# Kernel tuning notes

Hardware: AMD Instinct MI355X
Metric: run time of the kernel (lower is better)

Reference implementation:

```python
import jax, jax.numpy as jnp
import numpy as np

T = 2.0          # temperature (hardcoded to 2 in the torch module)
EPSILON = 0.1    # sinkhorn entropic regularization
N_ITERS = 10     # sinkhorn_loss default n_iters
CLIP_MAX = 10.0  # torch.clamp(Wxy, max=10.0)
EPS = 1e-8
LOSS_SCALE = 0.001


def setup_inputs() -> dict:
    key = jax.random.key(0)
    k1, k2 = jax.random.split(key)
    B, N, D = 4, 256, 512
    y_s = jax.random.normal(k1, (B, N, D), dtype=jnp.float32)
    y_t = jax.random.normal(k2, (B, N, D), dtype=jnp.float32)
    return {"y_s": y_s, "y_t": y_t}


def _sinkhorn_sample(x, y):
    # x, y: [N, D] probability rows. L1 cost matrix [N, N].
    W = jnp.sum(jnp.abs(x[:, None, :] - y[None, :, :]), axis=-1)
    Wc = jnp.minimum(W, CLIP_MAX)
    K = jnp.exp(-Wc / EPSILON) + EPS  # x = x + 1e-8 before normalization

    def step(P, _):
        P = P / jnp.maximum(jnp.sum(P, axis=1, keepdims=True), EPS)
        P = P / jnp.maximum(jnp.sum(P, axis=0, keepdims=True), EPS)
        return P, None

    P, _ = jax.lax.scan(step, K, None, length=N_ITERS)
    return jnp.sum(P * W)


def reference(y_s, y_t):
    p_s = jax.nn.softmax(y_s / T, axis=-1)
    p_t = jax.nn.softmax(y_t / T, axis=-1)
    losses = jax.vmap(_sinkhorn_sample)(p_s, p_t)  # [B]
    # emd_loss = sum_i 0.001 * loss_i; returned value = emd_loss / B
    return LOSS_SCALE * jnp.mean(losses)
```

## Files before the change

kernel.cpp:

```cpp
#include <hip/hip_runtime.h>

#define NB 4
#define NN 256
#define ND 512
#define NITER 10

typedef __attribute__((ext_vector_type(8))) unsigned short ushort8v;

__device__ __forceinline__ unsigned short f2bf(float x) {
  unsigned u = __float_as_uint(x);
  u += 0x7fffu + ((u >> 16) & 1u);
  return (unsigned short)(u >> 16);
}
__device__ __forceinline__ float bf2f(unsigned short h) {
  return __uint_as_float(((unsigned)h) << 16);
}

__global__ __launch_bounds__(256) void softmax_k(const float* __restrict__ ys,
                                                 const float* __restrict__ yt,
                                                 float* __restrict__ ps,
                                                 float* __restrict__ pt) {
  int bb = blockIdx.x;
  const float* src = (bb < NB * NN) ? ys : yt;
  float* dst       = (bb < NB * NN) ? ps : pt;
  int row = bb & (NB * NN - 1);
  const float* rp = src + (size_t)row * ND;
  float* wp = dst + (size_t)row * ND;
  int t = threadIdx.x;
  float a = rp[t];
  float b = rp[t + 256];
  float m = fmaxf(a, b);
  #pragma unroll
  for (int s = 1; s < 64; s <<= 1) m = fmaxf(m, __shfl_xor(m, s));
  __shared__ float red[4];
  int wid = t >> 6;
  if ((t & 63) == 0) red[wid] = m;
  __syncthreads();
  m = fmaxf(fmaxf(red[0], red[1]), fmaxf(red[2], red[3]));
  float e0 = expf((a - m) * 0.5f);
  float e1 = expf((b - m) * 0.5f);
  float ssum = e0 + e1;
  #pragma unroll
  for (int s = 1; s < 64; s <<= 1) ssum += __shfl_xor(ssum, s);
  __syncthreads();
  if ((t & 63) == 0) red[wid] = ssum;
  __syncthreads();
  ssum = red[0] + red[1] + red[2] + red[3];
  float inv = 1.0f / ssum;
  wp[t] = e0 * inv;
  wp[t + 256] = e1 * inv;
}

__global__ __launch_bounds__(256) void cost_k(const float* __restrict__ ps,
                                              const float* __restrict__ pt,
                                              float* __restrict__ W) {
  __shared__ float xs[32 * 512];
  __shared__ float ysh[32 * 512];
  int b  = blockIdx.z;
  int It = blockIdx.y * 32;
  int Jt = blockIdx.x * 32;
  int t = threadIdx.x;
  const float4* xg = reinterpret_cast<const float4*>(ps + ((size_t)b * NN + It) * ND);
  const float4* yg = reinterpret_cast<const float4*>(pt + ((size_t)b * NN + Jt) * ND);
  float4* xsv = reinterpret_cast<float4*>(xs);
  float4* ysv = reinterpret_cast<float4*>(ysh);
  #pragma unroll
  for (int s = 0; s < 16; ++s) {
    int idx = s * 256 + t;
    int r = idx >> 7;
    int q = idx & 127;
    int qs = q ^ ((r >> 1) & 7);
    xsv[r * 128 + qs] = xg[idx];
    ysv[r * 128 + qs] = yg[idx];
  }
  __syncthreads();
  int tx = t & 15, ty = t >> 4;
  int i0 = ty * 2, j0 = tx * 2;
  int sx = ty & 7;
  int sy = tx & 7;
  float a00 = 0.f, a01 = 0.f, a10 = 0.f, a11 = 0.f;
  for (int q = 0; q < 128; ++q) {
    float4 x0 = xsv[i0 * 128 + (q ^ sx)];
    float4 x1 = xsv[(i0 + 1) * 128 + (q ^ sx)];
    float4 y0 = ysv[j0 * 128 + (q ^ sy)];
    float4 y1 = ysv[(j0 + 1) * 128 + (q ^ sy)];
    a00 += fabsf(x0.x - y0.x) + fabsf(x0.y - y0.y) + fabsf(x0.z - y0.z) + fabsf(x0.w - y0.w);
    a01 += fabsf(x0.x - y1.x) + fabsf(x0.y - y1.y) + fabsf(x0.z - y1.z) + fabsf(x0.w - y1.w);
    a10 += fabsf(x1.x - y0.x) + fabsf(x1.y - y0.y) + fabsf(x1.z - y0.z) + fabsf(x1.w - y0.w);
    a11 += fabsf(x1.x - y1.x) + fabsf(x1.y - y1.y) + fabsf(x1.z - y1.z) + fabsf(x1.w - y1.w);
  }
  size_t base = ((size_t)b * NN + It + i0) * NN + Jt + j0;
  W[base]          = a00;  W[base + 1]      = a01;
  W[base + NN]     = a10;  W[base + NN + 1] = a11;
}

__global__ __launch_bounds__(1024) void sink_k(const float* __restrict__ Wg,
                                               float* __restrict__ losses) {
  __shared__ __align__(16) unsigned short Kl[NN * NN];
  __shared__ __align__(16) float u[NN];
  __shared__ __align__(16) float v[NN];
  __shared__ __align__(16) float scr[8 * NN];
  int b = blockIdx.x;
  int t = threadIdx.x;
  const float4* W4 = reinterpret_cast<const float4*>(Wg + (size_t)b * NN * NN);

  #pragma unroll
  for (int s = 0; s < 16; ++s) {
    int q = s * 1024 + t;
    int e = q * 4;
    int i = e >> 8;
    int j = e & 255;
    float4 w4 = W4[q];
    float k0 = __expf(fminf(w4.x, 10.0f) * -10.0f) + 1e-8f;
    float k1 = __expf(fminf(w4.y, 10.0f) * -10.0f) + 1e-8f;
    float k2 = __expf(fminf(w4.z, 10.0f) * -10.0f) + 1e-8f;
    float k3 = __expf(fminf(w4.w, 10.0f) * -10.0f) + 1e-8f;
    int pj = j ^ ((i & 7) << 3);
    ushort4 kk;
    kk.x = f2bf(k0); kk.y = f2bf(k1); kk.z = f2bf(k2); kk.w = f2bf(k3);
    *reinterpret_cast<ushort4*>(&Kl[i * 256 + pj]) = kk;
  }
  if (t < NN) { u[t] = 1.0f; v[t] = 1.0f; }
  __syncthreads();

  for (int it = 0; it < NITER; ++it) {
    {
      int i = t & 255, c = t >> 8;
      const int rowb = i * 256;
      const int sw = (i & 7) << 3;
      float acc = 0.0f;
      #pragma unroll
      for (int q = 0; q < 8; ++q) {
        int j0 = c * 64 + q * 8;
        float4 va = *reinterpret_cast<const float4*>(&v[j0]);
        float4 vb = *reinterpret_cast<const float4*>(&v[j0 + 4]);
        ushort8v k8 = *reinterpret_cast<const ushort8v*>(&Kl[rowb + (j0 ^ sw)]);
        acc += bf2f(k8[0]) * va.x + bf2f(k8[1]) * va.y +
               bf2f(k8[2]) * va.z + bf2f(k8[3]) * va.w +
               bf2f(k8[4]) * vb.x + bf2f(k8[5]) * vb.y +
               bf2f(k8[6]) * vb.z + bf2f(k8[7]) * vb.w;
      }
      scr[c * 256 + i] = acc;
    }
    __syncthreads();
    if (t < NN) {
      float r = scr[t] + scr[256 + t] + scr[512 + t] + scr[768 + t];
      float uo = u[t];
      u[t] = uo / fmaxf(uo * r, 1e-8f);
    }
    __syncthreads();
    {
      int j2 = t & 127, c = t >> 7;
      float acc0 = 0.0f, acc1 = 0.0f;
      #pragma unroll
      for (int q = 0; q < 8; ++q) {
        int ib = c * 32 + q * 4;
        float4 uq = *reinterpret_cast<const float4*>(&u[ib]);
        {
          int i = ib + 0;
          unsigned dw = *reinterpret_cast<const unsigned*>(&Kl[i * 256 + ((2 * j2) ^ ((i & 7) << 3))]);
          acc0 += __uint_as_float(dw << 16) * uq.x;
          acc1 += __uint_as_float(dw & 0xffff0000u) * uq.x;
        }
        {
          int i = ib + 1;
          unsigned dw = *reinterpret_cast<const unsigned*>(&Kl[i * 256 + ((2 * j2) ^ ((i & 7) << 3))]);
          acc0 += __uint_as_float(dw << 16) * uq.y;
          acc1 += __uint_as_float(dw & 0xffff0000u) * uq.y;
        }
        {
          int i = ib + 2;
          unsigned dw = *reinterpret_cast<const unsigned*>(&Kl[i * 256 + ((2 * j2) ^ ((i & 7) << 3))]);
          acc0 += __uint_as_float(dw << 16) * uq.z;
          acc1 += __uint_as_float(dw & 0xffff0000u) * uq.z;
        }
        {
          int i = ib + 3;
          unsigned dw = *reinterpret_cast<const unsigned*>(&Kl[i * 256 + ((2 * j2) ^ ((i & 7) << 3))]);
          acc0 += __uint_as_float(dw << 16) * uq.w;
          acc1 += __uint_as_float(dw & 0xffff0000u) * uq.w;
        }
      }
      *reinterpret_cast<float2*>(&scr[c * 256 + 2 * j2]) = make_float2(acc0, acc1);
    }
    __syncthreads();
    if (t < NN) {
      float s0 = 0.0f;
      #pragma unroll
      for (int c = 0; c < 8; ++c) s0 += scr[c * 256 + t];
      float vo = v[t];
      v[t] = vo / fmaxf(vo * s0, 1e-8f);
    }
    __syncthreads();
  }

  float acc = 0.0f;
  #pragma unroll
  for (int s = 0; s < 16; ++s) {
    int q = s * 1024 + t;
    int e = q * 4;
    int i = e >> 8;
    int j = e & 255;
    float4 w4 = W4[q];
    int pj = j ^ ((i & 7) << 3);
    ushort4 k4 = *reinterpret_cast<const ushort4*>(&Kl[i * 256 + pj]);
    float4 v4 = *reinterpret_cast<const float4*>(&v[j]);
    float ui = u[i];
    acc += ui * (bf2f(k4.x) * v4.x * w4.x + bf2f(k4.y) * v4.y * w4.y +
                 bf2f(k4.z) * v4.z * w4.z + bf2f(k4.w) * v4.w * w4.w);
  }
  #pragma unroll
  for (int s = 1; s < 64; s <<= 1) acc += __shfl_xor(acc, s);
  __syncthreads();
  if ((t & 63) == 0) scr[t >> 6] = acc;
  __syncthreads();
  if (t == 0) {
    float tot = 0.0f;
    #pragma unroll
    for (int w = 0; w < 16; ++w) tot += scr[w];
    losses[b] = tot;
  }
}

__global__ void final_k(const float* __restrict__ losses, float* __restrict__ out) {
  if (threadIdx.x == 0 && blockIdx.x == 0) {
    out[0] = 0.001f * 0.25f * (losses[0] + losses[1] + losses[2] + losses[3]);
  }
}

extern "C" void kernel_launch(void* const* d_in, const int* in_sizes, int n_in,
                              void* d_out, int out_size, void* d_ws, size_t ws_size,
                              hipStream_t stream) {
  const float* ys = (const float*)d_in[0];
  const float* yt = (const float*)d_in[1];
  float* ws = (float*)d_ws;
  float* ps = ws;
  float* pt = ps + (size_t)NB * NN * ND;
  float* W  = pt + (size_t)NB * NN * ND;
  float* losses = W + (size_t)NB * NN * NN;
  float* out = (float*)d_out;

  softmax_k<<<2 * NB * NN, 256, 0, stream>>>(ys, yt, ps, pt);
  cost_k<<<dim3(8, 8, NB), 256, 0, stream>>>(ps, pt, W);
  sink_k<<<NB, 1024, 0, stream>>>(W, losses);
  final_k<<<1, 64, 0, stream>>>(losses, out);
}
```

Measured before the change: 112.7 us.

## Store softmax and cost matrix in fp16, drop final kernel via atomicAdd

Softmax outputs and the L1 cost matrix are now stored as fp16 instead of fp32, halving global and LDS traffic in the cost and sinkhorn kernels. The cost kernel uses 8-wide half vectors with a rotation-based LDS swizzle. The column-sum pass in sinkhorn is repartitioned into 16 chunks of 4 columns each. The final reduction kernel is removed: output is zeroed in softmax and each sinkhorn block atomically adds its scaled loss. The trade-off is fp16 rounding of probabilities and of cost values up to ~2, which perturbs exp(-10W) and the loss sum.

```diff
diff --git a/kernel.cpp b/kernel.cpp
--- a/kernel.cpp
+++ b/kernel.cpp
@@ -5,7 +5,10 @@
 #define ND 512
 #define NITER 10
 
+typedef _Float16 half_t;
 typedef __attribute__((ext_vector_type(8))) unsigned short ushort8v;
+typedef __attribute__((ext_vector_type(8))) _Float16 half8v;
+typedef __attribute__((ext_vector_type(2))) _Float16 half2v;
 
 __device__ __forceinline__ unsigned short f2bf(float x) {
   unsigned u = __float_as_uint(x);
@@ -18,14 +21,16 @@
 
 __global__ __launch_bounds__(256) void softmax_k(const float* __restrict__ ys,
                                                  const float* __restrict__ yt,
-                                                 float* __restrict__ ps,
-                                                 float* __restrict__ pt) {
+                                                 half_t* __restrict__ ps,
+                                                 half_t* __restrict__ pt,
+                                                 float* __restrict__ out) {
   int bb = blockIdx.x;
+  if (bb == 0 && threadIdx.x == 0) out[0] = 0.0f;
   const float* src = (bb < NB * NN) ? ys : yt;
-  float* dst       = (bb < NB * NN) ? ps : pt;
+  half_t* dst      = (bb < NB * NN) ? ps : pt;
   int row = bb & (NB * NN - 1);
   const float* rp = src + (size_t)row * ND;
-  float* wp = dst + (size_t)row * ND;
+  half_t* wp = dst + (size_t)row * ND;
   int t = threadIdx.x;
   float a = rp[t];
   float b = rp[t + 256];
@@ -47,78 +52,88 @@
   __syncthreads();
   ssum = red[0] + red[1] + red[2] + red[3];
   float inv = 1.0f / ssum;
-  wp[t] = e0 * inv;
-  wp[t + 256] = e1 * inv;
-}
-
-__global__ __launch_bounds__(256) void cost_k(const float* __restrict__ ps,
-                                              const float* __restrict__ pt,
-                                              float* __restrict__ W) {
-  __shared__ float xs[32 * 512];
-  __shared__ float ysh[32 * 512];
+  wp[t]       = (half_t)(e0 * inv);
+  wp[t + 256] = (half_t)(e1 * inv);
+}
+
+__global__ __launch_bounds__(256) void cost_k(const half_t* __restrict__ ps,
+                                              const half_t* __restrict__ pt,
+                                              half_t* __restrict__ W) {
+  __shared__ half_t xs[32 * 512];
+  __shared__ half_t ysh[32 * 512];
   int b  = blockIdx.z;
   int It = blockIdx.y * 32;
   int Jt = blockIdx.x * 32;
   int t = threadIdx.x;
-  const float4* xg = reinterpret_cast<const float4*>(ps + ((size_t)b * NN + It) * ND);
-  const float4* yg = reinterpret_cast<const float4*>(pt + ((size_t)b * NN + Jt) * ND);
-  float4* xsv = reinterpret_cast<float4*>(xs);
-  float4* ysv = reinterpret_cast<float4*>(ysh);
-  #pragma unroll
-  for (int s = 0; s < 16; ++s) {
-    int idx = s * 256 + t;
-    int r = idx >> 7;
-    int q = idx & 127;
-    int qs = q ^ ((r >> 1) & 7);
-    xsv[r * 128 + qs] = xg[idx];
-    ysv[r * 128 + qs] = yg[idx];
+  const half8v* xg = reinterpret_cast<const half8v*>(ps + ((size_t)b * NN + It) * ND);
+  const half8v* yg = reinterpret_cast<const half8v*>(pt + ((size_t)b * NN + Jt) * ND);
+  half8v* xsv = reinterpret_cast<half8v*>(xs);
+  half8v* ysv = reinterpret_cast<half8v*>(ysh);
+  #pragma unroll
+  for (int s = 0; s < 8; ++s) {
+    int qidx = s * 256 + t;
+    int r = qidx >> 6;
+    int q = qidx & 63;
+    int rot = (r + (r >> 3)) & 7;
+    int dst = r * 64 + ((q + rot) & 63);
+    xsv[dst] = xg[qidx];
+    ysv[dst] = yg[qidx];
   }
   __syncthreads();
   int tx = t & 15, ty = t >> 4;
-  int i0 = ty * 2, j0 = tx * 2;
-  int sx = ty & 7;
-  int sy = tx & 7;
+  int i0 = 2 * ty, j0 = 2 * tx;
+  int rx0 = (i0 + (i0 >> 3)) & 7;
+  int rx1 = ((i0 + 1) + ((i0 + 1) >> 3)) & 7;
+  int ry0 = (j0 + (j0 >> 3)) & 7;
+  int ry1 = ((j0 + 1) + ((j0 + 1) >> 3)) & 7;
   float a00 = 0.f, a01 = 0.f, a10 = 0.f, a11 = 0.f;
-  for (int q = 0; q < 128; ++q) {
-    float4 x0 = xsv[i0 * 128 + (q ^ sx)];
-    float4 x1 = xsv[(i0 + 1) * 128 + (q ^ sx)];
-    float4 y0 = ysv[j0 * 128 + (q ^ sy)];
-    float4 y1 = ysv[(j0 + 1) * 128 + (q ^ sy)];
-    a00 += fabsf(x0.x - y0.x) + fabsf(x0.y - y0.y) + fabsf(x0.z - y0.z) + fabsf(x0.w - y0.w);
-    a01 += fabsf(x0.x - y1.x) + fabsf(x0.y - y1.y) + fabsf(x0.z - y1.z) + fabsf(x0.w - y1.w);
-    a10 += fabsf(x1.x - y0.x) + fabsf(x1.y - y0.y) + fabsf(x1.z - y0.z) + fabsf(x1.w - y0.w);
-    a11 += fabsf(x1.x - y1.x) + fabsf(x1.y - y1.y) + fabsf(x1.z - y1.z) + fabsf(x1.w - y1.w);
-  }
-  size_t base = ((size_t)b * NN + It + i0) * NN + Jt + j0;
-  W[base]          = a00;  W[base + 1]      = a01;
-  W[base + NN]     = a10;  W[base + NN + 1] = a11;
-}
-
-__global__ __launch_bounds__(1024) void sink_k(const float* __restrict__ Wg,
-                                               float* __restrict__ losses) {
+  #pragma unroll 4
+  for (int qq = 0; qq < 64; ++qq) {
+    half8v x0 = xsv[i0 * 64 + ((qq + rx0) & 63)];
+    half8v x1 = xsv[(i0 + 1) * 64 + ((qq + rx1) & 63)];
+    half8v y0 = ysv[j0 * 64 + ((qq + ry0) & 63)];
+    half8v y1 = ysv[(j0 + 1) * 64 + ((qq + ry1) & 63)];
+    #pragma unroll
+    for (int e = 0; e < 8; ++e) {
+      float xf0 = (float)x0[e], xf1 = (float)x1[e];
+      float yf0 = (float)y0[e], yf1 = (float)y1[e];
+      a00 += fabsf(xf0 - yf0);
+      a01 += fabsf(xf0 - yf1);
+      a10 += fabsf(xf1 - yf0);
+      a11 += fabsf(xf1 - yf1);
+    }
+  }
+  half_t* wb = W + ((size_t)b * NN + It + i0) * NN + Jt + j0;
+  half2v w0; w0[0] = (half_t)a00; w0[1] = (half_t)a01;
+  half2v w1; w1[0] = (half_t)a10; w1[1] = (half_t)a11;
+  *reinterpret_cast<half2v*>(wb)      = w0;
+  *reinterpret_cast<half2v*>(wb + NN) = w1;
+}
+
+__global__ __launch_bounds__(1024) void sink_k(const half_t* __restrict__ Wg,
+                                               float* __restrict__ out) {
   __shared__ __align__(16) unsigned short Kl[NN * NN];
   __shared__ __align__(16) float u[NN];
   __shared__ __align__(16) float v[NN];
-  __shared__ __align__(16) float scr[8 * NN];
+  __shared__ __align__(16) float scr[16 * NN];
   int b = blockIdx.x;
   int t = threadIdx.x;
-  const float4* W4 = reinterpret_cast<const float4*>(Wg + (size_t)b * NN * NN);
-
-  #pragma unroll
-  for (int s = 0; s < 16; ++s) {
-    int q = s * 1024 + t;
-    int e = q * 4;
+  const half8v* W8 = reinterpret_cast<const half8v*>(Wg + (size_t)b * NN * NN);
+
+  #pragma unroll
+  for (int s = 0; s < 8; ++s) {
+    int q8 = s * 1024 + t;
+    int e = q8 * 8;
     int i = e >> 8;
     int j = e & 255;
-    float4 w4 = W4[q];
-    float k0 = __expf(fminf(w4.x, 10.0f) * -10.0f) + 1e-8f;
-    float k1 = __expf(fminf(w4.y, 10.0f) * -10.0f) + 1e-8f;
-    float k2 = __expf(fminf(w4.z, 10.0f) * -10.0f) + 1e-8f;
-    float k3 = __expf(fminf(w4.w, 10.0f) * -10.0f) + 1e-8f;
-    int pj = j ^ ((i & 7) << 3);
-    ushort4 kk;
-    kk.x = f2bf(k0); kk.y = f2bf(k1); kk.z = f2bf(k2); kk.w = f2bf(k3);
-    *reinterpret_cast<ushort4*>(&Kl[i * 256 + pj]) = kk;
+    half8v w8 = W8[q8];
+    ushort8v kk;
+    #pragma unroll
+    for (int r = 0; r < 8; ++r) {
+      float kf = __expf(fminf((float)w8[r], 10.0f) * -10.0f) + 1e-8f;
+      kk[r] = f2bf(kf);
+    }
+    *reinterpret_cast<ushort8v*>(&Kl[i * 256 + (j ^ ((i & 7) << 3))]) = kk;
   }
   if (t < NN) { u[t] = 1.0f; v[t] = 1.0f; }
   __syncthreads();
@@ -150,44 +165,45 @@
     }
     __syncthreads();
     {
-      int j2 = t & 127, c = t >> 7;
-      float acc0 = 0.0f, acc1 = 0.0f;
+      int j4 = t & 63, c = t >> 6;
+      int jc = 4 * j4;
+      float acc0 = 0.f, acc1 = 0.f, acc2 = 0.f, acc3 = 0.f;
       #pragma unroll
-      for (int q = 0; q < 8; ++q) {
-        int ib = c * 32 + q * 4;
+      for (int q4 = 0; q4 < 4; ++q4) {
+        int ib = c * 16 + q4 * 4;
         float4 uq = *reinterpret_cast<const float4*>(&u[ib]);
         {
           int i = ib + 0;
-          unsigned dw = *reinterpret_cast<const unsigned*>(&Kl[i * 256 + ((2 * j2) ^ ((i & 7) << 3))]);
-          acc0 += __uint_as_float(dw << 16) * uq.x;
-          acc1 += __uint_as_float(dw & 0xffff0000u) * uq.x;
+          ushort4 k4 = *reinterpret_cast<const ushort4*>(&Kl[i * 256 + (jc ^ ((i & 7) << 3))]);
+          acc0 += bf2f(k4.x) * uq.x; acc1 += bf2f(k4.y) * uq.x;
+          acc2 += bf2f(k4.z) * uq.x; acc3 += bf2f(k4.w) * uq.x;
         }
         {
           int i = ib + 1;
-          unsigned dw = *reinterpret_cast<const unsigned*>(&Kl[i * 256 + ((2 * j2) ^ ((i & 7) << 3))]);
-          acc0 += __uint_as_float(dw << 16) * uq.y;
-          acc1 += __uint_as_float(dw & 0xffff0000u) * uq.y;
+          ushort4 k4 = *reinterpret_cast<const ushort4*>(&Kl[i * 256 + (jc ^ ((i & 7) << 3))]);
+          acc0 += bf2f(k4.x) * uq.y; acc1 += bf2f(k4.y) * uq.y;
+          acc2 += bf2f(k4.z) * uq.y; acc3 += bf2f(k4.w) * uq.y;
         }
         {
           int i = ib + 2;
-          unsigned dw = *reinterpret_cast<const unsigned*>(&Kl[i * 256 + ((2 * j2) ^ ((i & 7) << 3))]);
-          acc0 += __uint_as_float(dw << 16) * uq.z;
-          acc1 += __uint_as_float(dw & 0xffff0000u) * uq.z;
+          ushort4 k4 = *reinterpret_cast<const ushort4*>(&Kl[i * 256 + (jc ^ ((i & 7) << 3))]);
+          acc0 += bf2f(k4.x) * uq.z; acc1 += bf2f(k4.y) * uq.z;
+          acc2 += bf2f(k4.z) * uq.z; acc3 += bf2f(k4.w) * uq.z;
         }
         {
           int i = ib + 3;
-          unsigned dw = *reinterpret_cast<const unsigned*>(&Kl[i * 256 + ((2 * j2) ^ ((i & 7) << 3))]);
-          acc0 += __uint_as_float(dw << 16) * uq.w;
-          acc1 += __uint_as_float(dw & 0xffff0000u) * uq.w;
+          ushort4 k4 = *reinterpret_cast<const ushort4*>(&Kl[i * 256 + (jc ^ ((i & 7) << 3))]);
+          acc0 += bf2f(k4.x) * uq.w; acc1 += bf2f(k4.y) * uq.w;
+          acc2 += bf2f(k4.z) * uq.w; acc3 += bf2f(k4.w) * uq.w;
         }
       }
-      *reinterpret_cast<float2*>(&scr[c * 256 + 2 * j2]) = make_float2(acc0, acc1);
+      *reinterpret_cast<float4*>(&scr[c * 256 + jc]) = make_float4(acc0, acc1, acc2, acc3);
     }
     __syncthreads();
     if (t < NN) {
       float s0 = 0.0f;
       #pragma unroll
-      for (int c = 0; c < 8; ++c) s0 += scr[c * 256 + t];
+      for (int c = 0; c < 16; ++c) s0 += scr[c * 256 + t];
       float vo = v[t];
       v[t] = vo / fmaxf(vo * s0, 1e-8f);
     }
@@ -196,18 +212,20 @@
 
   float acc = 0.0f;
   #pragma unroll
-  for (int s = 0; s < 16; ++s) {
-    int q = s * 1024 + t;
-    int e = q * 4;
+  for (int s = 0; s < 8; ++s) {
+    int q8 = s * 1024 + t;
+    int e = q8 * 8;
     int i = e >> 8;
     int j = e & 255;
-    float4 w4 = W4[q];
-    int pj = j ^ ((i & 7) << 3);
-    ushort4 k4 = *reinterpret_cast<const ushort4*>(&Kl[i * 256 + pj]);
-    float4 v4 = *reinterpret_cast<const float4*>(&v[j]);
+    half8v w8 = W8[q8];
+    ushort8v k8 = *reinterpret_cast<const ushort8v*>(&Kl[i * 256 + (j ^ ((i & 7) << 3))]);
     float ui = u[i];
-    acc += ui * (bf2f(k4.x) * v4.x * w4.x + bf2f(k4.y) * v4.y * w4.y +
-                 bf2f(k4.z) * v4.z * w4.z + bf2f(k4.w) * v4.w * w4.w);
+    float4 v0 = *reinterpret_cast<const float4*>(&v[j]);
+    float4 v1 = *reinterpret_cast<const float4*>(&v[j + 4]);
+    acc += ui * (bf2f(k8[0]) * v0.x * (float)w8[0] + bf2f(k8[1]) * v0.y * (float)w8[1] +
+                 bf2f(k8[2]) * v0.z * (float)w8[2] + bf2f(k8[3]) * v0.w * (float)w8[3] +
+                 bf2f(k8[4]) * v1.x * (float)w8[4] + bf2f(k8[5]) * v1.y * (float)w8[5] +
+                 bf2f(k8[6]) * v1.z * (float)w8[6] + bf2f(k8[7]) * v1.w * (float)w8[7]);
   }
   #pragma unroll
   for (int s = 1; s < 64; s <<= 1) acc += __shfl_xor(acc, s);
@@ -218,13 +236,7 @@
     float tot = 0.0f;
     #pragma unroll
     for (int w = 0; w < 16; ++w) tot += scr[w];
-    losses[b] = tot;
-  }
-}
-
-__global__ void final_k(const float* __restrict__ losses, float* __restrict__ out) {
-  if (threadIdx.x == 0 && blockIdx.x == 0) {
-    out[0] = 0.001f * 0.25f * (losses[0] + losses[1] + losses[2] + losses[3]);
+    atomicAdd(out, 2.5e-4f * tot);
   }
 }
 
@@ -233,15 +245,12 @@
                               hipStream_t stream) {
   const float* ys = (const float*)d_in[0];
   const float* yt = (const float*)d_in[1];
-  float* ws = (float*)d_ws;
-  float* ps = ws;
-  float* pt = ps + (size_t)NB * NN * ND;
-  float* W  = pt + (size_t)NB * NN * ND;
-  float* losses = W + (size_t)NB * NN * NN;
+  half_t* ps = (half_t*)d_ws;
+  half_t* pt = ps + (size_t)NB * NN * ND;
+  half_t* W  = pt + (size_t)NB * NN * ND;
   float* out = (float*)d_out;
 
-  softmax_k<<<2 * NB * NN, 256, 0, stream>>>(ys, yt, ps, pt);
+  softmax_k<<<2 * NB * NN, 256, 0, stream>>>(ys, yt, ps, pt, out);
   cost_k<<<dim3(8, 8, NB), 256, 0, stream>>>(ps, pt, W);
-  sink_k<<<NB, 1024, 0, stream>>>(W, losses);
-  final_k<<<1, 64, 0, stream>>>(losses, out);
-}
+  sink_k<<<NB, 1024, 0, stream>>>(W, out);
+}
```

Result: faster. 107.9 us (-4.2%).
